# Kernel optimization log

Hardware: AMD Instinct MI355X
Metric: run time of the kernel (lower is better)

The kernel has to match this reference:

```python
import jax, jax.numpy as jnp
import numpy as np

B, T, D, R = 4, 1024, 512, 64
SLOTS = (1024, 256, 64)
K = 16


def _layernorm(x, g, b, eps=1e-5):
    m = jnp.mean(x, axis=-1, keepdims=True)
    v = jnp.mean(jnp.square(x - m), axis=-1, keepdims=True)
    return (x - m) * jax.lax.rsqrt(v + eps) * g + b


def _signed_softmax(x):
    # signed softmax over the slot axis: sign(x) * softmax(|x|)
    return jnp.sign(x) * jax.nn.softmax(jnp.abs(x), axis=-1)


def _transition_delta(src_val, src_state, dst_val, W, k, n_dst):
    # Low-rank bilinear routing: logits [B, Ns, Nd]
    q = jnp.einsum('bsd,dr->bsr', src_val, W[0])
    kk = jnp.einsum('bnd,dr->bnr', dst_val, W[1])
    logits = jnp.einsum('bsr,bnr->bsn', q, kk) / jnp.sqrt(jnp.float32(W.shape[-1]))
    v, idx = jax.lax.top_k(logits, k)                      # [B, Ns, k]
    w = jnp.sign(v) * jax.nn.softmax(jnp.abs(v), axis=-1)  # signed_abs_softmax over selected edges
    c = w * jax.nn.softplus(src_state)[:, :, None]         # state-weighted edge coefficients [B, Ns, k]
    d = src_val.shape[-1]
    edge_val = (c[..., None] * src_val[:, :, None, :]).reshape(src_val.shape[0], -1, d)
    idx_f = idx.reshape(idx.shape[0], -1)
    cf = c.reshape(c.shape[0], -1)

    def _scatter(i, ev, cc):
        dv = jnp.zeros((n_dst, d), src_val.dtype).at[i].add(ev)
        ds = jnp.zeros((n_dst,), src_val.dtype).at[i].add(cc)
        return ds, dv

    return jax.vmap(_scatter)(idx_f, edge_val, cf)


def _apply_delta(state, val, dstate, dval, g, b):
    # residual merge, then constrain: signed softmax state + LayerNorm values
    return _signed_softmax(state + dstate), _layernorm(val + dval, g, b)


def setup_inputs() -> dict:
    key = jax.random.key(0)
    ks = jax.random.split(key, 20)
    rn = lambda k, s, sc=1.0: jax.random.normal(k, s, jnp.float32) * sc
    return {
        'tok_val': rn(ks[0], (B, T, D)),
        'tok_state': rn(ks[1], (B, T)),
        'mem_state0': rn(ks[2], (B, SLOTS[0]), 0.02),
        'mem_val0': rn(ks[3], (B, SLOTS[0], D), 0.02),
        'mem_state1': rn(ks[4], (B, SLOTS[1]), 0.02),
        'mem_val1': rn(ks[5], (B, SLOTS[1], D), 0.02),
        'mem_state2': rn(ks[6], (B, SLOTS[2]), 0.02),
        'mem_val2': rn(ks[7], (B, SLOTS[2], D), 0.02),
        'write_route': rn(ks[8], (1, 2, D, R), 0.05),
        'prop_route': rn(ks[9], (3, 2, D, R), 0.05),
        'level_route': rn(ks[10], (2, 2, D, R), 0.05),
        'skip_route': rn(ks[11], (2, 2, D, R), 0.05),
        'skip_gates': jnp.full((2,), -1.5, jnp.float32),
        'ln_gamma': jnp.ones((3, D), jnp.float32),
        'ln_beta': jnp.zeros((3, D), jnp.float32),
        'read_route': rn(ks[12], (3, 2, D, R), 0.05),
        'read_proj': rn(ks[13], (3, D, D), 0.02),
        'read_gates': jnp.zeros((3,), jnp.float32),
        'topk': K,
    }


def reference(tok_val, tok_state, mem_state0, mem_val0, mem_state1, mem_val1,
              mem_state2, mem_val2, write_route, prop_route, level_route,
              skip_route, skip_gates, ln_gamma, ln_beta, read_route, read_proj,
              read_gates, topk):
    k = int(topk)
    S0, S1, S2 = mem_state0.shape[1], mem_state1.shape[1], mem_state2.shape[1]

    # --- level 0: token write + pairwise propagation ---
    ds, dv = _transition_delta(tok_val, tok_state, mem_val0, write_route[0], min(k, S0), S0)
    s0, v0 = _apply_delta(mem_state0, mem_val0, ds, dv, ln_gamma[0], ln_beta[0])
    ds, dv = _transition_delta(v0, s0, v0, prop_route[0], min(k, S0), S0)
    s0, v0 = _apply_delta(s0, v0, ds, dv, ln_gamma[0], ln_beta[0])

    # --- level 1: transition from level 0, gated skip from tokens, propagation ---
    ds, dv = _transition_delta(v0, s0, mem_val1, level_route[0], min(k, S1), S1)
    s1, v1 = _apply_delta(mem_state1, mem_val1, ds, dv, ln_gamma[1], ln_beta[1])
    g = jax.nn.sigmoid(skip_gates[0])
    ds, dv = _transition_delta(tok_val, tok_state, v1, skip_route[0], min(k, S1), S1)
    s1, v1 = _apply_delta(s1, v1, g * ds, g * dv, ln_gamma[1], ln_beta[1])
    ds, dv = _transition_delta(v1, s1, v1, prop_route[1], min(k, S1), S1)
    s1, v1 = _apply_delta(s1, v1, ds, dv, ln_gamma[1], ln_beta[1])

    # --- level 2: transition from level 1, gated skip from level 0, propagation ---
    ds, dv = _transition_delta(v1, s1, mem_val2, level_route[1], min(k, S2), S2)
    s2, v2 = _apply_delta(mem_state2, mem_val2, ds, dv, ln_gamma[2], ln_beta[2])
    g = jax.nn.sigmoid(skip_gates[1])
    ds, dv = _transition_delta(v0, s0, v2, skip_route[1], min(k, S2), S2)
    s2, v2 = _apply_delta(s2, v2, g * ds, g * dv, ln_gamma[2], ln_beta[2])
    ds, dv = _transition_delta(v2, s2, v2, prop_route[2], min(k, S2), S2)
    s2, v2 = _apply_delta(s2, v2, ds, dv, ln_gamma[2], ln_beta[2])

    # --- read: tokens attend over each memory level, gated projected residual ---
    out = tok_val
    for l, mv in enumerate((v0, v1, v2)):
        q = jnp.einsum('btd,dr->btr', tok_val, read_route[l, 0])
        kk = jnp.einsum('bnd,dr->bnr', mv, read_route[l, 1])
        logits = jnp.einsum('btr,bnr->btn', q, kk) / jnp.sqrt(jnp.float32(R))
        attn = jax.nn.softmax(logits, axis=-1)
        r = jnp.einsum('btn,bnd->btd', attn, mv)
        out = out + jax.nn.sigmoid(read_gates[l]) * jnp.einsum('btd,de->bte', r, read_proj[l])
    return out
```

## Files before the change

### kernel.cpp

```cpp
#include <hip/hip_runtime.h>
#include <math.h>

typedef __attribute__((ext_vector_type(8))) short short8;
typedef __attribute__((ext_vector_type(4))) float floatx4;

static __device__ __forceinline__ short f2bf(float f) {
    union { float f; unsigned u; } c; c.f = f;
    unsigned r = c.u + 0x7FFF + ((c.u >> 16) & 1);
    return (short)(r >> 16);
}

__launch_bounds__(256)
__global__ void gemm_f32_nt_kernel(const float* __restrict__ A, const float* __restrict__ B,
                                   float* __restrict__ C, int M, int N, int K,
                                   long sA, long sB, long sC, float alpha)
{
    __shared__ float As[32][68];
    __shared__ float Bs[32][68];
    const float* Ab = A + (long)blockIdx.z * sA;
    const float* Bb = B + (long)blockIdx.z * sB;
    float* Cb = C + (long)blockIdx.z * sC;
    int m0 = blockIdx.x * 64, n0 = blockIdx.y * 64;
    int t = threadIdx.x;
    int tx = t & 15, ty = t >> 4;
    float acc[4][4] = {};

    for (int k0 = 0; k0 < K; k0 += 32) {
        {
            int m = t >> 3;
            int kk = (t & 7) * 4;
#pragma unroll
            for (int h = 0; h < 2; ++h) {
                float4 v = *(const float4*)&Ab[(long)(m0 + m + 32 * h) * K + k0 + kk];
                As[kk + 0][m + 32 * h] = v.x; As[kk + 1][m + 32 * h] = v.y;
                As[kk + 2][m + 32 * h] = v.z; As[kk + 3][m + 32 * h] = v.w;
            }
        }
        {
            int n = t >> 3;
            int kk = (t & 7) * 4;
#pragma unroll
            for (int h = 0; h < 2; ++h) {
                float4 v = *(const float4*)&Bb[(long)(n0 + n + 32 * h) * K + k0 + kk];
                Bs[kk + 0][n + 32 * h] = v.x; Bs[kk + 1][n + 32 * h] = v.y;
                Bs[kk + 2][n + 32 * h] = v.z; Bs[kk + 3][n + 32 * h] = v.w;
            }
        }
        __syncthreads();
#pragma unroll 4
        for (int k = 0; k < 32; ++k) {
            float4 a = *(const float4*)&As[k][ty * 4];
            float4 b = *(const float4*)&Bs[k][tx * 4];
            float av[4] = { a.x, a.y, a.z, a.w };
            float bv[4] = { b.x, b.y, b.z, b.w };
#pragma unroll
            for (int i = 0; i < 4; ++i)
#pragma unroll
                for (int j = 0; j < 4; ++j) acc[i][j] += av[i] * bv[j];
        }
        __syncthreads();
    }
#pragma unroll
    for (int i = 0; i < 4; ++i) {
        float4 r;
        r.x = alpha * acc[i][0]; r.y = alpha * acc[i][1];
        r.z = alpha * acc[i][2]; r.w = alpha * acc[i][3];
        *(float4*)&Cb[(long)(m0 + ty * 4 + i) * N + n0 + tx * 4] = r;
    }
}

__launch_bounds__(256)
__global__ void proj_splitk_kernel(const float* __restrict__ Aq, const float* __restrict__ Ak,
                                   const float* __restrict__ Wq, const float* __restrict__ Wk,
                                   float* __restrict__ part,
                                   int Mq, int Mk, long sAq, long sAk, int Bn)
{
    __shared__ float As[32][68];
    __shared__ float Bs[32][68];
    int mqT = Mq >> 6;
    int xt = blockIdx.x, s = blockIdx.y, b = blockIdx.z;
    const float* A; const float* W; int row0, orow;
    if (xt < mqT) { A = Aq + (long)b * sAq; W = Wq; row0 = xt * 64; orow = row0; }
    else { A = Ak + (long)b * sAk; W = Wk; row0 = (xt - mqT) * 64; orow = Mq + row0; }
    int t = threadIdx.x, tx = t & 15, ty = t >> 4;
    float acc[4][4] = {};
    int kbase = s * 64;

    for (int k0 = kbase; k0 < kbase + 64; k0 += 32) {
        {
            int m = t >> 3;
            int kk = (t & 7) * 4;
#pragma unroll
            for (int h = 0; h < 2; ++h) {
                float4 v = *(const float4*)&A[(long)(row0 + m + 32 * h) * 512 + k0 + kk];
                As[kk + 0][m + 32 * h] = v.x; As[kk + 1][m + 32 * h] = v.y;
                As[kk + 2][m + 32 * h] = v.z; As[kk + 3][m + 32 * h] = v.w;
            }
        }
        {
            int kk = t >> 3;
            int nn = (t & 7) * 8;
            float4 v0 = *(const float4*)&W[(long)(k0 + kk) * 64 + nn];
            float4 v1 = *(const float4*)&W[(long)(k0 + kk) * 64 + nn + 4];
            *(float4*)&Bs[kk][nn] = v0;
            *(float4*)&Bs[kk][nn + 4] = v1;
        }
        __syncthreads();
#pragma unroll 4
        for (int k = 0; k < 32; ++k) {
            float4 a = *(const float4*)&As[k][ty * 4];
            float4 b2 = *(const float4*)&Bs[k][tx * 4];
            float av[4] = { a.x, a.y, a.z, a.w };
            float bv[4] = { b2.x, b2.y, b2.z, b2.w };
#pragma unroll
            for (int i = 0; i < 4; ++i)
#pragma unroll
                for (int j = 0; j < 4; ++j) acc[i][j] += av[i] * bv[j];
        }
        __syncthreads();
    }
    long base = ((long)(s * Bn + b) * (Mq + Mk) + orow) * 64;
#pragma unroll
    for (int i = 0; i < 4; ++i)
        *(float4*)&part[base + (long)(ty * 4 + i) * 64 + tx * 4] =
            make_float4(acc[i][0], acc[i][1], acc[i][2], acc[i][3]);
}

__launch_bounds__(256)
__global__ void proj_reduce_kernel(const float* __restrict__ part,
                                   float* __restrict__ qout, float* __restrict__ kout,
                                   int Mq, int Mk, int Bn)
{
    int idx = blockIdx.x * 256 + threadIdx.x;
    int size4b = (Mq + Mk) * 16;
    int total4 = Bn * size4b;
    if (idx >= total4) return;
    const float4* p4 = (const float4*)part;
    long stride4 = (long)total4;
    float4 s = p4[idx];
#pragma unroll
    for (int ss = 1; ss < 8; ++ss) {
        float4 v = p4[ss * stride4 + idx];
        s.x += v.x; s.y += v.y; s.z += v.z; s.w += v.w;
    }
    int b = idx / size4b;
    int rem = idx - b * size4b;
    int r = rem >> 4;
    int c4 = rem & 15;
    if (r < Mq) ((float4*)qout)[((long)b * Mq + r) * 16 + c4] = s;
    else        ((float4*)kout)[((long)b * Mk + (r - Mq)) * 16 + c4] = s;
}

__launch_bounds__(256)
__global__ void gemm_mfma_kernel(const float* __restrict__ A, const unsigned short* __restrict__ Bt,
                                 float* __restrict__ C, int M, int N, int K,
                                 long sA, long sBt, long sC,
                                 float alpha, const float* __restrict__ gate, int gateIdx,
                                 float beta, const float* __restrict__ initC)
{
    __shared__ short As[2048];
    __shared__ short Bs[2048];
    const float* Ab = A + (long)blockIdx.z * sA;
    const unsigned short* Bb = Bt + (long)blockIdx.z * sBt;
    float* Cb = C + (long)blockIdx.z * sC;
    const float* Ib = initC ? initC + (long)blockIdx.z * sC : nullptr;
    int m0 = blockIdx.x * 64, n0 = blockIdx.y * 64;
    int t = threadIdx.x, wave = t >> 6, lane = t & 63;
    int sr = wave * 16 + (lane & 15);
    int sk = (lane >> 4) * 8;
    floatx4 acc[4] = {};

    for (int k0 = 0; k0 < K; k0 += 32) {
        const float* ap = &Ab[(long)(m0 + sr) * K + k0 + sk];
        float4 f0 = *(const float4*)ap;
        float4 f1 = *(const float4*)(ap + 4);
        short8 av;
        av[0] = f2bf(f0.x); av[1] = f2bf(f0.y); av[2] = f2bf(f0.z); av[3] = f2bf(f0.w);
        av[4] = f2bf(f1.x); av[5] = f2bf(f1.y); av[6] = f2bf(f1.z); av[7] = f2bf(f1.w);
        short8 bv = *(const short8*)&Bb[(long)(n0 + sr) * K + k0 + sk];
        ((short8*)As)[t] = av;
        ((short8*)Bs)[t] = bv;
        __syncthreads();
        short8 bf = ((short8*)Bs)[wave * 64 + lane];
#pragma unroll
        for (int mt = 0; mt < 4; ++mt) {
            short8 af = ((short8*)As)[mt * 64 + lane];
            acc[mt] = __builtin_amdgcn_mfma_f32_16x16x32_bf16(af, bf, acc[mt], 0, 0, 0);
        }
        __syncthreads();
    }
    float a = alpha;
    if (gate) a *= 1.f / (1.f + expf(-gate[gateIdx]));
    int col = n0 + wave * 16 + (lane & 15);
#pragma unroll
    for (int mt = 0; mt < 4; ++mt) {
#pragma unroll
        for (int r = 0; r < 4; ++r) {
            int row = m0 + mt * 16 + (lane >> 4) * 4 + r;
            long off = (long)row * N + col;
            float v = a * acc[mt][r];
            if (Ib) v += Ib[off];
            else if (beta != 0.f) v += Cb[off];
            Cb[off] = v;
        }
    }
}

__global__ void transpose_bf16_kernel(const float* __restrict__ in, unsigned short* __restrict__ out,
                                      int Rr, int Cc, long sIn, long sOut)
{
    __shared__ float tile[32][33];
    const float* I = in + (long)blockIdx.z * sIn;
    unsigned short* O = out + (long)blockIdx.z * sOut;
    int c0 = blockIdx.x * 32, r0 = blockIdx.y * 32;
    int tx = threadIdx.x, ty = threadIdx.y;
#pragma unroll
    for (int i = 0; i < 32; i += 8)
        tile[ty + i][tx] = I[(long)(r0 + ty + i) * Cc + c0 + tx];
    __syncthreads();
#pragma unroll
    for (int i = 0; i < 32; i += 8)
        O[(long)(c0 + ty + i) * Rr + r0 + tx] = (unsigned short)f2bf(tile[tx][ty + i]);
}

template<int CNT>
__launch_bounds__(256)
__global__ void topk_coeff_kernel(const float* __restrict__ logits,
                                  const float* __restrict__ state,
                                  int* __restrict__ idx_out, float* __restrict__ c_out,
                                  int* __restrict__ cnt, int nsLog, int Nd)
{
    int wave = threadIdx.x >> 6, lane = threadIdx.x & 63;
    long row = (long)blockIdx.x * 4 + wave;
    const float* L = logits + row * Nd;
    float vreg[CNT];
    if (CNT >= 4) {
#pragma unroll
        for (int q = 0; q < CNT / 4; ++q) {
            float4 v = *(const float4*)&L[lane * CNT + q * 4];
            vreg[q * 4 + 0] = v.x; vreg[q * 4 + 1] = v.y;
            vreg[q * 4 + 2] = v.z; vreg[q * 4 + 3] = v.w;
        }
    } else {
#pragma unroll
        for (int tt = 0; tt < CNT; ++tt) vreg[tt] = L[lane * CNT + tt];
    }

    float m = 0.f, sum = 0.f;
    float myv = 0.f; int myi = 0;
#pragma unroll
    for (int it = 0; it < 16; ++it) {
        float best = -INFINITY; int bidx = 0x7fffffff;
#pragma unroll
        for (int tt = 0; tt < CNT; ++tt) {
            if (vreg[tt] > best) { best = vreg[tt]; bidx = lane * CNT + tt; }
        }
#pragma unroll
        for (int off = 32; off; off >>= 1) {
            float ov = __shfl_down(best, off);
            int   oi = __shfl_down(bidx, off);
            if (ov > best || (ov == best && oi < bidx)) { best = ov; bidx = oi; }
        }
        best = __shfl(best, 0);
        bidx = __shfl(bidx, 0);
        if (it == lane) { myv = best; myi = bidx; }
        float ab = fabsf(best);
        float nm = fmaxf(m, ab);
        sum = sum * expf(m - nm) + expf(ab - nm);
        m = nm;
#pragma unroll
        for (int tt = 0; tt < CNT; ++tt)
            if (lane * CNT + tt == bidx) vreg[tt] = -INFINITY;
    }
    if (lane < 16) {
        float st = state[row];
        float sp = fmaxf(st, 0.f) + log1pf(expf(-fabsf(st)));
        float sgn = (myv > 0.f) ? 1.f : ((myv < 0.f) ? -1.f : 0.f);
        float w = expf(fabsf(myv) - m) / sum;
        c_out[row * 16 + lane] = sgn * w * sp;
        idx_out[row * 16 + lane] = myi;
        int b = (int)(row >> nsLog);
        atomicAdd(&cnt[b * Nd + myi], 1);
    }
}

__launch_bounds__(256)
__global__ void scan_kernel(int* __restrict__ cnt, int* __restrict__ offs, int N)
{
    __shared__ int sums[256];
    int t = threadIdx.x;
    int chunk = N >> 8;
    int base = t * chunk;
    int lc[16];
    int s = 0;
    for (int i = 0; i < chunk; ++i) { lc[i] = cnt[base + i]; s += lc[i]; }
    sums[t] = s;
    __syncthreads();
    for (int off = 1; off < 256; off <<= 1) {
        int v = (t >= off) ? sums[t - off] : 0;
        __syncthreads();
        sums[t] += v;
        __syncthreads();
    }
    int run = sums[t] - s;
    for (int i = 0; i < chunk; ++i) {
        offs[base + i] = run;
        run += lc[i];
        cnt[base + i] = 0;
    }
    if (t == 255) offs[N] = run;
}

__launch_bounds__(256)
__global__ void fill_edges_kernel(const int* __restrict__ idx, const int* __restrict__ offs,
                                  int* __restrict__ cursor, int* __restrict__ elist,
                                  int nsShift, int Nd, int E)
{
    int e = blockIdx.x * 256 + threadIdx.x;
    if (e >= E) return;
    int b = e >> nsShift;
    int d = b * Nd + idx[e];
    int pos = offs[d] + atomicAdd(&cursor[d], 1);
    elist[pos] = e;
}

#define ECHUNK 512
__launch_bounds__(256)
__global__ void gather_dv_kernel(const float* __restrict__ src_val, const float* __restrict__ c,
                                 const int* __restrict__ elist, const int* __restrict__ offs,
                                 float* __restrict__ dv, float* __restrict__ ds,
                                 int* __restrict__ cursor, int nsShift)
{
    __shared__ float sc[ECHUNK];
    __shared__ int   srow[ECHUNK];
    __shared__ float part[4][512];
    __shared__ float pcs[4];
    long row = blockIdx.x;
    int t = threadIdx.x, w = t >> 6, lane = t & 63;
    int e0 = offs[row], e1 = offs[row + 1];
    int mask = (1 << nsShift) - 1;
    int cb = lane * 8;
    float a[8] = {};
    float cs = 0.f;

    for (int cstart = e0; cstart < e1; cstart += ECHUNK) {
        int cnt = min(e1 - cstart, ECHUNK);
        for (int i = t; i < cnt; i += 256) {
            int e = elist[cstart + i];
            sc[i] = c[e];
            int b = e >> nsShift;
            int s = (e & mask) >> 4;
            srow[i] = (b << (nsShift - 4)) + s;
        }
        __syncthreads();
        int j = w;
        for (; j + 12 < cnt; j += 16) {
            float c0 = sc[j], c1 = sc[j + 4], c2 = sc[j + 8], c3 = sc[j + 12];
            const float* p0 = src_val + ((long)srow[j]      << 9) + cb;
            const float* p1 = src_val + ((long)srow[j + 4]  << 9) + cb;
            const float* p2 = src_val + ((long)srow[j + 8]  << 9) + cb;
            const float* p3 = src_val + ((long)srow[j + 12] << 9) + cb;
            float4 x00 = *(const float4*)p0,       x01 = *(const float4*)(p0 + 4);
            float4 x10 = *(const float4*)p1,       x11 = *(const float4*)(p1 + 4);
            float4 x20 = *(const float4*)p2,       x21 = *(const float4*)(p2 + 4);
            float4 x30 = *(const float4*)p3,       x31 = *(const float4*)(p3 + 4);
            a[0] += c0 * x00.x + c1 * x10.x + c2 * x20.x + c3 * x30.x;
            a[1] += c0 * x00.y + c1 * x10.y + c2 * x20.y + c3 * x30.y;
            a[2] += c0 * x00.z + c1 * x10.z + c2 * x20.z + c3 * x30.z;
            a[3] += c0 * x00.w + c1 * x10.w + c2 * x20.w + c3 * x30.w;
            a[4] += c0 * x01.x + c1 * x11.x + c2 * x21.x + c3 * x31.x;
            a[5] += c0 * x01.y + c1 * x11.y + c2 * x21.y + c3 * x31.y;
            a[6] += c0 * x01.z + c1 * x11.z + c2 * x21.z + c3 * x31.z;
            a[7] += c0 * x01.w + c1 * x11.w + c2 * x21.w + c3 * x31.w;
            cs += c0 + c1 + c2 + c3;
        }
        for (; j < cnt; j += 4) {
            float cv = sc[j];
            const float* p = src_val + ((long)srow[j] << 9) + cb;
            float4 x0 = *(const float4*)p, x1 = *(const float4*)(p + 4);
            a[0] += cv * x0.x; a[1] += cv * x0.y; a[2] += cv * x0.z; a[3] += cv * x0.w;
            a[4] += cv * x1.x; a[5] += cv * x1.y; a[6] += cv * x1.z; a[7] += cv * x1.w;
            cs += cv;
        }
        __syncthreads();
    }
#pragma unroll
    for (int i = 0; i < 8; ++i) part[w][cb + i] = a[i];
    if (lane == 0) pcs[w] = cs;
    __syncthreads();
    float r0 = part[0][t] + part[1][t] + part[2][t] + part[3][t];
    float r1 = part[0][t + 256] + part[1][t + 256] + part[2][t + 256] + part[3][t + 256];
    dv[(row << 9) + t]       = r0;
    dv[(row << 9) + t + 256] = r1;
    if (t == 0) { ds[row] = pcs[0] + pcs[1] + pcs[2] + pcs[3]; cursor[row] = 0; }
}

__launch_bounds__(256)
__global__ void apply_fused_kernel(const float* __restrict__ s_in, const float* __restrict__ ds,
                                   float* __restrict__ s_out,
                                   const float* __restrict__ v_in, const float* __restrict__ dv,
                                   float* __restrict__ v_out,
                                   const float* __restrict__ gamma, const float* __restrict__ beta,
                                   int Nd, int Bn,
                                   const float* __restrict__ gatePtr, int gateIdx)
{
    __shared__ float sh[1024];
    __shared__ float red[4];
    int t = threadIdx.x;
    float gate = 1.f;
    if (gatePtr) gate = 1.f / (1.f + expf(-gatePtr[gateIdx]));
    int nLN = gridDim.x - Bn;

    if ((int)blockIdx.x < nLN) {
        long row = blockIdx.x;
        const float* vi  = v_in + (row << 9);
        const float* dvi = dv   + (row << 9);
        float x0 = vi[t]       + gate * dvi[t];
        float x1 = vi[t + 256] + gate * dvi[t + 256];
        float s = x0 + x1;
        for (int off = 32; off; off >>= 1) s += __shfl_down(s, off);
        if ((t & 63) == 0) red[t >> 6] = s;
        __syncthreads();
        float mean = (red[0] + red[1] + red[2] + red[3]) * (1.f / 512.f);
        float d0 = x0 - mean, d1 = x1 - mean;
        float ss = d0 * d0 + d1 * d1;
        for (int off = 32; off; off >>= 1) ss += __shfl_down(ss, off);
        __syncthreads();
        if ((t & 63) == 0) red[t >> 6] = ss;
        __syncthreads();
        float var = (red[0] + red[1] + red[2] + red[3]) * (1.f / 512.f);
        float rstd = rsqrtf(var + 1e-5f);
        float* vo = v_out + (row << 9);
        vo[t]       = d0 * rstd * gamma[t]       + beta[t];
        vo[t + 256] = d1 * rstd * gamma[t + 256] + beta[t + 256];
    } else {
        int b = blockIdx.x - nLN;
        float lmax = 0.f;
        for (int i = t; i < Nd; i += 256) {
            float x = s_in[b * Nd + i] + gate * ds[b * Nd + i];
            sh[i] = x;
            lmax = fmaxf(lmax, fabsf(x));
        }
        for (int off = 32; off; off >>= 1) lmax = fmaxf(lmax, __shfl_down(lmax, off));
        if ((t & 63) == 0) red[t >> 6] = lmax;
        __syncthreads();
        float bmax = fmaxf(fmaxf(red[0], red[1]), fmaxf(red[2], red[3]));
        float lsum = 0.f;
        for (int i = t; i < Nd; i += 256) lsum += expf(fabsf(sh[i]) - bmax);
        for (int off = 32; off; off >>= 1) lsum += __shfl_down(lsum, off);
        __syncthreads();
        if ((t & 63) == 0) red[t >> 6] = lsum;
        __syncthreads();
        float inv = 1.f / (red[0] + red[1] + red[2] + red[3]);
        for (int i = t; i < Nd; i += 256) {
            float x = sh[i];
            float sgn = (x > 0.f) ? 1.f : ((x < 0.f) ? -1.f : 0.f);
            s_out[b * Nd + i] = sgn * expf(fabsf(x) - bmax) * inv;
        }
    }
}

__launch_bounds__(256)
__global__ void softmax_rows_kernel(float* __restrict__ logits, int Nd)
{
    __shared__ float red[4];
    long row = blockIdx.x;
    int t = threadIdx.x;
    float* L = logits + row * (long)Nd;
    float lmax = -INFINITY;
    for (int i = t; i < Nd; i += 256) lmax = fmaxf(lmax, L[i]);
    for (int off = 32; off; off >>= 1) lmax = fmaxf(lmax, __shfl_down(lmax, off));
    if ((t & 63) == 0) red[t >> 6] = lmax;
    __syncthreads();
    float bmax = fmaxf(fmaxf(red[0], red[1]), fmaxf(red[2], red[3]));
    float lsum = 0.f;
    for (int i = t; i < Nd; i += 256) lsum += expf(L[i] - bmax);
    for (int off = 32; off; off >>= 1) lsum += __shfl_down(lsum, off);
    __syncthreads();
    if ((t & 63) == 0) red[t >> 6] = lsum;
    __syncthreads();
    float inv = 1.f / (red[0] + red[1] + red[2] + red[3]);
    for (int i = t; i < Nd; i += 256) L[i] = expf(L[i] - bmax) * inv;
}

extern "C" void kernel_launch(void* const* d_in, const int* in_sizes, int n_in,
                              void* d_out, int out_size, void* d_ws, size_t ws_size,
                              hipStream_t stream)
{
    const int Bn = 4, T = 1024, D = 512, R = 64;
    const int S0 = 1024, S1 = 256, S2 = 64;
    const long RT = (long)D * R;

    const float* tok_val    = (const float*)d_in[0];
    const float* tok_state  = (const float*)d_in[1];
    const float* mem_state0 = (const float*)d_in[2];
    const float* mem_val0   = (const float*)d_in[3];
    const float* mem_state1 = (const float*)d_in[4];
    const float* mem_val1   = (const float*)d_in[5];
    const float* mem_state2 = (const float*)d_in[6];
    const float* mem_val2   = (const float*)d_in[7];
    const float* write_route= (const float*)d_in[8];
    const float* prop_route = (const float*)d_in[9];
    const float* level_route= (const float*)d_in[10];
    const float* skip_route = (const float*)d_in[11];
    const float* skip_gates = (const float*)d_in[12];
    const float* ln_gamma   = (const float*)d_in[13];
    const float* ln_beta    = (const float*)d_in[14];
    const float* read_route = (const float*)d_in[15];
    const float* read_proj  = (const float*)d_in[16];
    const float* read_gates = (const float*)d_in[17];
    float* out = (float*)d_out;

    float* p = (float*)d_ws;
    float* v0 = p;  p += (long)Bn * S0 * D;
    float* s0 = p;  p += Bn * S0;
    float* v1 = p;  p += (long)Bn * S1 * D;
    float* s1 = p;  p += Bn * S1;
    float* v2 = p;  p += (long)Bn * S2 * D;
    float* s2 = p;  p += Bn * S2;
    float* qb = p;  p += (long)Bn * T * R;
    float* kb = p;  p += (long)Bn * S0 * R;
    float* lb = p;  p += (long)Bn * T * S0;
    float* cb = p;  p += (long)Bn * T * 16;
    int*   ib = (int*)p; p += (long)Bn * T * 16;
    float* dvb = p; p += (long)Bn * S0 * D;
    float* dsb = p; p += Bn * S0;
    float* rb = p;  p += (long)Bn * T * D;
    int* cntb  = (int*)p; p += Bn * S0;
    int* curb  = (int*)p; p += Bn * S0;
    int* offsb = (int*)p; p += Bn * S0 + 1;
    int* elistb= (int*)p; p += (long)Bn * T * 16;
    unsigned short* projT = (unsigned short*)p; p += (3 * (long)D * D) / 2 + 4;
    float* partb = p; p += 8L * Bn * (T + S0) * R;
    unsigned short* mvT = (unsigned short*)dvb;

    auto proj = [&](const float* Aq, const float* Ak, const float* Wq, const float* Wk,
                    int Mq, int Mk, long sAq, long sAk, float* qout, float* kout) {
        proj_splitk_kernel<<<dim3((Mq + Mk) / 64, 8, Bn), 256, 0, stream>>>(
            Aq, Ak, Wq, Wk, partb, Mq, Mk, sAq, sAk, Bn);
        int total4 = Bn * (Mq + Mk) * 16;
        proj_reduce_kernel<<<(total4 + 255) / 256, 256, 0, stream>>>(
            partb, qout, kout, Mq, Mk, Bn);
    };

    hipMemsetAsync(cntb, 0, (size_t)2 * Bn * S0 * sizeof(int), stream);

    auto trans = [&](const float* sv, const float* ss, const float* dval,
                     const float* W, int Ns, int Nd) {
        proj(sv, dval, W, W + RT, Ns, Nd, (long)Ns * D, (long)Nd * D, qb, kb);
        gemm_f32_nt_kernel<<<dim3(Ns / 64, Nd / 64, Bn), 256, 0, stream>>>(
            qb, kb, lb, Ns, Nd, R, (long)Ns * R, (long)Nd * R, (long)Ns * Nd, 0.125f);
        int nsLog = 31 - __builtin_clz((unsigned)Ns);
        int nsShift = nsLog + 4;
        int rowBlocks = Bn * Ns / 4;
        if (Nd == 1024)
            topk_coeff_kernel<16><<<rowBlocks, 256, 0, stream>>>(lb, ss, ib, cb, cntb, nsLog, Nd);
        else if (Nd == 256)
            topk_coeff_kernel<4><<<rowBlocks, 256, 0, stream>>>(lb, ss, ib, cb, cntb, nsLog, Nd);
        else
            topk_coeff_kernel<1><<<rowBlocks, 256, 0, stream>>>(lb, ss, ib, cb, cntb, nsLog, Nd);
        int E = Bn * Ns * 16;
        scan_kernel<<<1, 256, 0, stream>>>(cntb, offsb, Bn * Nd);
        fill_edges_kernel<<<(E + 255) / 256, 256, 0, stream>>>(ib, offsb, curb, elistb,
                                                               nsShift, Nd, E);
        gather_dv_kernel<<<Bn * Nd, 256, 0, stream>>>(sv, cb, elistb, offsb, dvb, dsb,
                                                      curb, nsShift);
    };
    auto apply = [&](const float* sin, float* sout, const float* vin, float* vout,
                     int Nd, int lvl, const float* gptr, int gidx) {
        apply_fused_kernel<<<Bn * Nd + Bn, 256, 0, stream>>>(
            sin, dsb, sout, vin, dvb, vout,
            ln_gamma + lvl * D, ln_beta + lvl * D, Nd, Bn, gptr, gidx);
    };

    trans(tok_val, tok_state, mem_val0, write_route, T, S0);
    apply(mem_state0, s0, mem_val0, v0, S0, 0, nullptr, 0);
    trans(v0, s0, v0, prop_route + 0 * 2 * RT, S0, S0);
    apply(s0, s0, v0, v0, S0, 0, nullptr, 0);

    trans(v0, s0, mem_val1, level_route + 0 * 2 * RT, S0, S1);
    apply(mem_state1, s1, mem_val1, v1, S1, 1, nullptr, 0);
    trans(tok_val, tok_state, v1, skip_route + 0 * 2 * RT, T, S1);
    apply(s1, s1, v1, v1, S1, 1, skip_gates, 0);
    trans(v1, s1, v1, prop_route + 1 * 2 * RT, S1, S1);
    apply(s1, s1, v1, v1, S1, 1, nullptr, 0);

    trans(v1, s1, mem_val2, level_route + 1 * 2 * RT, S1, S2);
    apply(mem_state2, s2, mem_val2, v2, S2, 2, nullptr, 0);
    trans(v0, s0, v2, skip_route + 1 * 2 * RT, S0, S2);
    apply(s2, s2, v2, v2, S2, 2, skip_gates, 1);
    trans(v2, s2, v2, prop_route + 2 * 2 * RT, S2, S2);
    apply(s2, s2, v2, v2, S2, 2, nullptr, 0);

    transpose_bf16_kernel<<<dim3(D / 32, D / 32, 3), dim3(32, 8), 0, stream>>>(
        read_proj, projT, D, D, (long)D * D, (long)D * D);
    const float* mvs[3] = { v0, v1, v2 };
    const int nds[3] = { S0, S1, S2 };
    for (int l = 0; l < 3; ++l) {
        const float* mv = mvs[l];
        int Nd = nds[l];
        proj(tok_val, mv, read_route + (long)l * 2 * RT, read_route + (long)l * 2 * RT + RT,
             T, Nd, (long)T * D, (long)Nd * D, qb, kb);
        gemm_f32_nt_kernel<<<dim3(T / 64, Nd / 64, Bn), 256, 0, stream>>>(
            qb, kb, lb, T, Nd, R, (long)T * R, (long)Nd * R, (long)T * Nd, 0.125f);
        softmax_rows_kernel<<<Bn * T, 256, 0, stream>>>(lb, Nd);
        transpose_bf16_kernel<<<dim3(D / 32, Nd / 32, Bn), dim3(32, 8), 0, stream>>>(
            mv, mvT, Nd, D, (long)Nd * D, (long)D * Nd);
        gemm_mfma_kernel<<<dim3(T / 64, D / 64, Bn), 256, 0, stream>>>(
            lb, mvT, rb, T, D, Nd, (long)T * Nd, (long)D * Nd, (long)T * D,
            1.f, nullptr, 0, 0.f, nullptr);
        gemm_mfma_kernel<<<dim3(T / 64, D / 64, Bn), 256, 0, stream>>>(
            rb, projT + (long)l * D * D, out, T, D, D,
            (long)T * D, 0, (long)T * D, 1.f, read_gates, l,
            1.f, (l == 0) ? tok_val : nullptr);
    }
}
```

Measured before the change: 930.4 us.

## Fuse routing logits into top-k and fuse gather with LayerNorm apply

```diff
diff --git a/kernel.cpp b/kernel.cpp
--- a/kernel.cpp
+++ b/kernel.cpp
@@ -225,25 +225,31 @@
 
 template<int CNT>
 __launch_bounds__(256)
-__global__ void topk_coeff_kernel(const float* __restrict__ logits,
-                                  const float* __restrict__ state,
-                                  int* __restrict__ idx_out, float* __restrict__ c_out,
-                                  int* __restrict__ cnt, int nsLog, int Nd)
+__global__ void logits_topk_kernel(const float* __restrict__ q, const float* __restrict__ k,
+                                   const float* __restrict__ state,
+                                   int* __restrict__ idx_out, float* __restrict__ c_out,
+                                   int* __restrict__ cnt, int nsLog, int Nd)
 {
     int wave = threadIdx.x >> 6, lane = threadIdx.x & 63;
     long row = (long)blockIdx.x * 4 + wave;
-    const float* L = logits + row * Nd;
+    int b = (int)(row >> nsLog);
+    const float* qr = q + row * 64;
+    const float* kbase = k + (long)b * Nd * 64;
+    float4 q4[16];
+#pragma unroll
+    for (int i = 0; i < 16; ++i) q4[i] = *(const float4*)&qr[i * 4];
+
     float vreg[CNT];
-    if (CNT >= 4) {
-#pragma unroll
-        for (int q = 0; q < CNT / 4; ++q) {
-            float4 v = *(const float4*)&L[lane * CNT + q * 4];
-            vreg[q * 4 + 0] = v.x; vreg[q * 4 + 1] = v.y;
-            vreg[q * 4 + 2] = v.z; vreg[q * 4 + 3] = v.w;
-        }
-    } else {
-#pragma unroll
-        for (int tt = 0; tt < CNT; ++tt) vreg[tt] = L[lane * CNT + tt];
+#pragma unroll
+    for (int tt = 0; tt < CNT; ++tt) {
+        const float* kr = kbase + (long)(lane * CNT + tt) * 64;
+        float s = 0.f;
+#pragma unroll
+        for (int i = 0; i < 16; ++i) {
+            float4 kv = *(const float4*)&kr[i * 4];
+            s += q4[i].x * kv.x + q4[i].y * kv.y + q4[i].z * kv.z + q4[i].w * kv.w;
+        }
+        vreg[tt] = s * 0.125f;
     }
 
     float m = 0.f, sum = 0.f;
@@ -279,7 +285,6 @@
         float w = expf(fabsf(myv) - m) / sum;
         c_out[row * 16 + lane] = sgn * w * sp;
         idx_out[row * 16 + lane] = myi;
-        int b = (int)(row >> nsLog);
         atomicAdd(&cnt[b * Nd + myi], 1);
     }
 }
@@ -326,15 +331,18 @@
 
 #define ECHUNK 512
 __launch_bounds__(256)
-__global__ void gather_dv_kernel(const float* __restrict__ src_val, const float* __restrict__ c,
+__global__ void gather_ln_kernel(const float* __restrict__ src_val, const float* __restrict__ c,
                                  const int* __restrict__ elist, const int* __restrict__ offs,
-                                 float* __restrict__ dv, float* __restrict__ ds,
-                                 int* __restrict__ cursor, int nsShift)
+                                 const float* __restrict__ v_in, float* __restrict__ v_out,
+                                 float* __restrict__ ds, int* __restrict__ cursor,
+                                 const float* __restrict__ gamma, const float* __restrict__ beta,
+                                 const float* __restrict__ gatePtr, int gateIdx, int nsShift)
 {
     __shared__ float sc[ECHUNK];
     __shared__ int   srow[ECHUNK];
     __shared__ float part[4][512];
     __shared__ float pcs[4];
+    __shared__ float red[4];
     long row = blockIdx.x;
     int t = threadIdx.x, w = t >> 6, lane = t & 63;
     int e0 = offs[row], e1 = offs[row + 1];
@@ -342,6 +350,8 @@
     int cb = lane * 8;
     float a[8] = {};
     float cs = 0.f;
+    float gate = 1.f;
+    if (gatePtr) gate = 1.f / (1.f + expf(-gatePtr[gateIdx]));
 
     for (int cstart = e0; cstart < e1; cstart += ECHUNK) {
         int cnt = min(e1 - cstart, ECHUNK);
@@ -390,73 +400,60 @@
     __syncthreads();
     float r0 = part[0][t] + part[1][t] + part[2][t] + part[3][t];
     float r1 = part[0][t + 256] + part[1][t + 256] + part[2][t + 256] + part[3][t + 256];
-    dv[(row << 9) + t]       = r0;
-    dv[(row << 9) + t + 256] = r1;
     if (t == 0) { ds[row] = pcs[0] + pcs[1] + pcs[2] + pcs[3]; cursor[row] = 0; }
-}
-
-__launch_bounds__(256)
-__global__ void apply_fused_kernel(const float* __restrict__ s_in, const float* __restrict__ ds,
-                                   float* __restrict__ s_out,
-                                   const float* __restrict__ v_in, const float* __restrict__ dv,
-                                   float* __restrict__ v_out,
-                                   const float* __restrict__ gamma, const float* __restrict__ beta,
-                                   int Nd, int Bn,
+
+    const float* vi = v_in + (row << 9);
+    float x0 = vi[t]       + gate * r0;
+    float x1 = vi[t + 256] + gate * r1;
+    float s = x0 + x1;
+    for (int off = 32; off; off >>= 1) s += __shfl_down(s, off);
+    if ((t & 63) == 0) red[t >> 6] = s;
+    __syncthreads();
+    float mean = (red[0] + red[1] + red[2] + red[3]) * (1.f / 512.f);
+    float d0 = x0 - mean, d1 = x1 - mean;
+    float ss = d0 * d0 + d1 * d1;
+    for (int off = 32; off; off >>= 1) ss += __shfl_down(ss, off);
+    __syncthreads();
+    if ((t & 63) == 0) red[t >> 6] = ss;
+    __syncthreads();
+    float var = (red[0] + red[1] + red[2] + red[3]) * (1.f / 512.f);
+    float rstd = rsqrtf(var + 1e-5f);
+    float* vo = v_out + (row << 9);
+    vo[t]       = d0 * rstd * gamma[t]       + beta[t];
+    vo[t + 256] = d1 * rstd * gamma[t + 256] + beta[t + 256];
+}
+
+__launch_bounds__(256)
+__global__ void apply_state_kernel(const float* __restrict__ s_in, const float* __restrict__ ds,
+                                   float* __restrict__ s_out, int Nd,
                                    const float* __restrict__ gatePtr, int gateIdx)
 {
     __shared__ float sh[1024];
     __shared__ float red[4];
-    int t = threadIdx.x;
+    int b = blockIdx.x, t = threadIdx.x;
     float gate = 1.f;
     if (gatePtr) gate = 1.f / (1.f + expf(-gatePtr[gateIdx]));
-    int nLN = gridDim.x - Bn;
-
-    if ((int)blockIdx.x < nLN) {
-        long row = blockIdx.x;
-        const float* vi  = v_in + (row << 9);
-        const float* dvi = dv   + (row << 9);
-        float x0 = vi[t]       + gate * dvi[t];
-        float x1 = vi[t + 256] + gate * dvi[t + 256];
-        float s = x0 + x1;
-        for (int off = 32; off; off >>= 1) s += __shfl_down(s, off);
-        if ((t & 63) == 0) red[t >> 6] = s;
-        __syncthreads();
-        float mean = (red[0] + red[1] + red[2] + red[3]) * (1.f / 512.f);
-        float d0 = x0 - mean, d1 = x1 - mean;
-        float ss = d0 * d0 + d1 * d1;
-        for (int off = 32; off; off >>= 1) ss += __shfl_down(ss, off);
-        __syncthreads();
-        if ((t & 63) == 0) red[t >> 6] = ss;
-        __syncthreads();
-        float var = (red[0] + red[1] + red[2] + red[3]) * (1.f / 512.f);
-        float rstd = rsqrtf(var + 1e-5f);
-        float* vo = v_out + (row << 9);
-        vo[t]       = d0 * rstd * gamma[t]       + beta[t];
-        vo[t + 256] = d1 * rstd * gamma[t + 256] + beta[t + 256];
-    } else {
-        int b = blockIdx.x - nLN;
-        float lmax = 0.f;
-        for (int i = t; i < Nd; i += 256) {
-            float x = s_in[b * Nd + i] + gate * ds[b * Nd + i];
-            sh[i] = x;
-            lmax = fmaxf(lmax, fabsf(x));
-        }
-        for (int off = 32; off; off >>= 1) lmax = fmaxf(lmax, __shfl_down(lmax, off));
-        if ((t & 63) == 0) red[t >> 6] = lmax;
-        __syncthreads();
-        float bmax = fmaxf(fmaxf(red[0], red[1]), fmaxf(red[2], red[3]));
-        float lsum = 0.f;
-        for (int i = t; i < Nd; i += 256) lsum += expf(fabsf(sh[i]) - bmax);
-        for (int off = 32; off; off >>= 1) lsum += __shfl_down(lsum, off);
-        __syncthreads();
-        if ((t & 63) == 0) red[t >> 6] = lsum;
-        __syncthreads();
-        float inv = 1.f / (red[0] + red[1] + red[2] + red[3]);
-        for (int i = t; i < Nd; i += 256) {
-            float x = sh[i];
-            float sgn = (x > 0.f) ? 1.f : ((x < 0.f) ? -1.f : 0.f);
-            s_out[b * Nd + i] = sgn * expf(fabsf(x) - bmax) * inv;
-        }
+    float lmax = 0.f;
+    for (int i = t; i < Nd; i += 256) {
+        float x = s_in[b * Nd + i] + gate * ds[b * Nd + i];
+        sh[i] = x;
+        lmax = fmaxf(lmax, fabsf(x));
+    }
+    for (int off = 32; off; off >>= 1) lmax = fmaxf(lmax, __shfl_down(lmax, off));
+    if ((t & 63) == 0) red[t >> 6] = lmax;
+    __syncthreads();
+    float bmax = fmaxf(fmaxf(red[0], red[1]), fmaxf(red[2], red[3]));
+    float lsum = 0.f;
+    for (int i = t; i < Nd; i += 256) lsum += expf(fabsf(sh[i]) - bmax);
+    for (int off = 32; off; off >>= 1) lsum += __shfl_down(lsum, off);
+    __syncthreads();
+    if ((t & 63) == 0) red[t >> 6] = lsum;
+    __syncthreads();
+    float inv = 1.f / (red[0] + red[1] + red[2] + red[3]);
+    for (int i = t; i < Nd; i += 256) {
+        float x = sh[i];
+        float sgn = (x > 0.f) ? 1.f : ((x < 0.f) ? -1.f : 0.f);
+        s_out[b * Nd + i] = sgn * expf(fabsf(x) - bmax) * inv;
     }
 }
 
@@ -512,27 +509,29 @@
     float* out = (float*)d_out;
 
     float* p = (float*)d_ws;
-    float* v0 = p;  p += (long)Bn * S0 * D;
-    float* s0 = p;  p += Bn * S0;
-    float* v1 = p;  p += (long)Bn * S1 * D;
-    float* s1 = p;  p += Bn * S1;
-    float* v2 = p;  p += (long)Bn * S2 * D;
-    float* s2 = p;  p += Bn * S2;
-    float* qb = p;  p += (long)Bn * T * R;
-    float* kb = p;  p += (long)Bn * S0 * R;
-    float* lb = p;  p += (long)Bn * T * S0;
-    float* cb = p;  p += (long)Bn * T * 16;
-    int*   ib = (int*)p; p += (long)Bn * T * 16;
-    float* dvb = p; p += (long)Bn * S0 * D;
+    float* v0  = p; p += (long)Bn * S0 * D;
+    float* v0b = p; p += (long)Bn * S0 * D;
+    float* s0  = p; p += Bn * S0;
+    float* v1  = p; p += (long)Bn * S1 * D;
+    float* v1b = p; p += (long)Bn * S1 * D;
+    float* s1  = p; p += Bn * S1;
+    float* v2  = p; p += (long)Bn * S2 * D;
+    float* v2b = p; p += (long)Bn * S2 * D;
+    float* s2  = p; p += Bn * S2;
+    float* qb  = p; p += (long)Bn * T * R;
+    float* kb  = p; p += (long)Bn * S0 * R;
+    float* lb  = p; p += (long)Bn * T * S0;
+    float* cbuf= p; p += (long)Bn * T * 16;
+    int*   ib  = (int*)p; p += (long)Bn * T * 16;
     float* dsb = p; p += Bn * S0;
-    float* rb = p;  p += (long)Bn * T * D;
+    float* rb  = p; p += (long)Bn * T * D;
     int* cntb  = (int*)p; p += Bn * S0;
     int* curb  = (int*)p; p += Bn * S0;
     int* offsb = (int*)p; p += Bn * S0 + 1;
     int* elistb= (int*)p; p += (long)Bn * T * 16;
     unsigned short* projT = (unsigned short*)p; p += (3 * (long)D * D) / 2 + 4;
+    unsigned short* mvT   = (unsigned short*)p; p += ((long)Bn * D * S0) / 2 + 4;
     float* partb = p; p += 8L * Bn * (T + S0) * R;
-    unsigned short* mvT = (unsigned short*)dvb;
 
     auto proj = [&](const float* Aq, const float* Ak, const float* Wq, const float* Wk,
                     int Mq, int Mk, long sAq, long sAk, float* qout, float* kout) {
@@ -546,55 +545,52 @@
     hipMemsetAsync(cntb, 0, (size_t)2 * Bn * S0 * sizeof(int), stream);
 
     auto trans = [&](const float* sv, const float* ss, const float* dval,
-                     const float* W, int Ns, int Nd) {
+                     const float* W, int Ns, int Nd,
+                     const float* v_in, float* v_out, const float* sin, float* sout,
+                     int lvl, const float* gptr, int gidx) {
         proj(sv, dval, W, W + RT, Ns, Nd, (long)Ns * D, (long)Nd * D, qb, kb);
-        gemm_f32_nt_kernel<<<dim3(Ns / 64, Nd / 64, Bn), 256, 0, stream>>>(
-            qb, kb, lb, Ns, Nd, R, (long)Ns * R, (long)Nd * R, (long)Ns * Nd, 0.125f);
         int nsLog = 31 - __builtin_clz((unsigned)Ns);
         int nsShift = nsLog + 4;
         int rowBlocks = Bn * Ns / 4;
         if (Nd == 1024)
-            topk_coeff_kernel<16><<<rowBlocks, 256, 0, stream>>>(lb, ss, ib, cb, cntb, nsLog, Nd);
+            logits_topk_kernel<16><<<rowBlocks, 256, 0, stream>>>(qb, kb, ss, ib, cbuf, cntb, nsLog, Nd);
         else if (Nd == 256)
-            topk_coeff_kernel<4><<<rowBlocks, 256, 0, stream>>>(lb, ss, ib, cb, cntb, nsLog, Nd);
+            logits_topk_kernel<4><<<rowBlocks, 256, 0, stream>>>(qb, kb, ss, ib, cbuf, cntb, nsLog, Nd);
         else
-            topk_coeff_kernel<1><<<rowBlocks, 256, 0, stream>>>(lb, ss, ib, cb, cntb, nsLog, Nd);
+            logits_topk_kernel<1><<<rowBlocks, 256, 0, stream>>>(qb, kb, ss, ib, cbuf, cntb, nsLog, Nd);
         int E = Bn * Ns * 16;
         scan_kernel<<<1, 256, 0, stream>>>(cntb, offsb, Bn * Nd);
         fill_edges_kernel<<<(E + 255) / 256, 256, 0, stream>>>(ib, offsb, curb, elistb,
                                                                nsShift, Nd, E);
-        gather_dv_kernel<<<Bn * Nd, 256, 0, stream>>>(sv, cb, elistb, offsb, dvb, dsb,
-                                                      curb, nsShift);
+        gather_ln_kernel<<<Bn * Nd, 256, 0, stream>>>(sv, cbuf, elistb, offsb,
+                                                      v_in, v_out, dsb, curb,
+                                                      ln_gamma + lvl * D, ln_beta + lvl * D,
+                                                      gptr, gidx, nsShift);
+        apply_state_kernel<<<Bn, 256, 0, stream>>>(sin, dsb, sout, Nd, gptr, gidx);
     };
-    auto apply = [&](const float* sin, float* sout, const float* vin, float* vout,
-                     int Nd, int lvl, const float* gptr, int gidx) {
-        apply_fused_kernel<<<Bn * Nd + Bn, 256, 0, stream>>>(
-            sin, dsb, sout, vin, dvb, vout,
-            ln_gamma + lvl * D, ln_beta + lvl * D, Nd, Bn, gptr, gidx);
-    };
-
-    trans(tok_val, tok_state, mem_val0, write_route, T, S0);
-    apply(mem_state0, s0, mem_val0, v0, S0, 0, nullptr, 0);
-    trans(v0, s0, v0, prop_route + 0 * 2 * RT, S0, S0);
-    apply(s0, s0, v0, v0, S0, 0, nullptr, 0);
-
-    trans(v0, s0, mem_val1, level_route + 0 * 2 * RT, S0, S1);
-    apply(mem_state1, s1, mem_val1, v1, S1, 1, nullptr, 0);
-    trans(tok_val, tok_state, v1, skip_route + 0 * 2 * RT, T, S1);
-    apply(s1, s1, v1, v1, S1, 1, skip_gates, 0);
-    trans(v1, s1, v1, prop_route + 1 * 2 * RT, S1, S1);
-    apply(s1, s1, v1, v1, S1, 1, nullptr, 0);
-
-    trans(v1, s1, mem_val2, level_route + 1 * 2 * RT, S1, S2);
-    apply(mem_state2, s2, mem_val2, v2, S2, 2, nullptr, 0);
-    trans(v0, s0, v2, skip_route + 1 * 2 * RT, S0, S2);
-    apply(s2, s2, v2, v2, S2, 2, skip_gates, 1);
-    trans(v2, s2, v2, prop_route + 2 * 2 * RT, S2, S2);
-    apply(s2, s2, v2, v2, S2, 2, nullptr, 0);
+
+    trans(tok_val, tok_state, mem_val0, write_route, T, S0,
+          mem_val0, v0, mem_state0, s0, 0, nullptr, 0);
+    trans(v0, s0, v0, prop_route + 0 * 2 * RT, S0, S0,
+          v0, v0b, s0, s0, 0, nullptr, 0);
+
+    trans(v0b, s0, mem_val1, level_route + 0 * 2 * RT, S0, S1,
+          mem_val1, v1, mem_state1, s1, 1, nullptr, 0);
+    trans(tok_val, tok_state, v1, skip_route + 0 * 2 * RT, T, S1,
+          v1, v1, s1, s1, 1, skip_gates, 0);
+    trans(v1, s1, v1, prop_route + 1 * 2 * RT, S1, S1,
+          v1, v1b, s1, s1, 1, nullptr, 0);
+
+    trans(v1b, s1, mem_val2, level_route + 1 * 2 * RT, S1, S2,
+          mem_val2, v2, mem_state2, s2, 2, nullptr, 0);
+    trans(v0b, s0, v2, skip_route + 1 * 2 * RT, S0, S2,
+          v2, v2, s2, s2, 2, skip_gates, 1);
+    trans(v2, s2, v2, prop_route + 2 * 2 * RT, S2, S2,
+          v2, v2b, s2, s2, 2, nullptr, 0);
 
     transpose_bf16_kernel<<<dim3(D / 32, D / 32, 3), dim3(32, 8), 0, stream>>>(
         read_proj, projT, D, D, (long)D * D, (long)D * D);
-    const float* mvs[3] = { v0, v1, v2 };
+    const float* mvs[3] = { v0b, v1b, v2b };
     const int nds[3] = { S0, S1, S2 };
     for (int l = 0; l < 3; ++l) {
         const float* mv = mvs[l];
```

Result: slower. 1.207 ms (+29.7%).
